# Performance work log

Hardware: AMD Instinct MI355X
Metric: run time of the kernel (lower is better)

The kernel has to match this reference:

```python
import jax, jax.numpy as jnp
import numpy as np
import math

B, C, N = 4, 128, 4096
GROUPS = 8
EPS = 1e-5


def setup_inputs() -> dict:
    key = jax.random.key(0)
    ks = jax.random.split(key, 7)
    x = jax.random.normal(ks[0], (B, C, N), dtype=jnp.float32)
    gn_w = jnp.ones((C,), dtype=jnp.float32)
    gn_b = jnp.zeros((C,), dtype=jnp.float32)
    # Conv1d with kernel_size=1 is a per-position linear map: weight [out, in]
    s_qkv = 1.0 / math.sqrt(C)
    w_qkv = jax.random.uniform(ks[1], (3 * C, C), jnp.float32, -s_qkv, s_qkv)
    b_qkv = jax.random.uniform(ks[2], (3 * C,), jnp.float32, -s_qkv, s_qkv)
    w_out = jax.random.uniform(ks[3], (C, C), jnp.float32, -s_qkv, s_qkv)
    b_out = jax.random.uniform(ks[4], (C,), jnp.float32, -s_qkv, s_qkv)
    return {"x": x, "gn_w": gn_w, "gn_b": gn_b, "w_qkv": w_qkv,
            "b_qkv": b_qkv, "w_out": w_out, "b_out": b_out}


def reference(x, gn_w, gn_b, w_qkv, b_qkv, w_out, b_out):
    b, c, n = x.shape
    # GroupNorm(8, c): normalize over (channels-in-group, n)
    xg = x.reshape(b, GROUPS, c // GROUPS, n)
    mean = jnp.mean(xg, axis=(2, 3), keepdims=True)
    var = jnp.var(xg, axis=(2, 3), keepdims=True)
    h = ((xg - mean) * jax.lax.rsqrt(var + EPS)).reshape(b, c, n)
    h = h * gn_w[None, :, None] + gn_b[None, :, None]
    # 1x1 conv QKV projection
    qkv = jnp.einsum('oc,bcn->bon', w_qkv, h) + b_qkv[None, :, None]
    q, k, v = jnp.split(qkv, 3, axis=1)  # each [b, c, n]
    scale = 1.0 / math.sqrt(c)
    attn = jax.nn.softmax(jnp.einsum('bci,bcj->bij', q, k) * scale, axis=-1)
    # h[b,c,i] = sum_j v[b,c,j] * attn[b,i,j]  (torch: bmm(v, attn^T))
    h2 = jnp.einsum('bcj,bij->bci', v, attn)
    out = jnp.einsum('oc,bcn->bon', w_out, h2) + b_out[None, :, None]
    return out + x
```

## Files before the change

kernel.cpp:

```cpp
#include <hip/hip_runtime.h>
#include <hip/hip_bf16.h>


#define CH 128
#define SEQ 4096
#define EPSV 1e-5f
#define QSCALE (0.08838834764831845f * 1.4426950408889634f)
#define SMAX 24.0f

typedef unsigned short u16;
typedef unsigned int u32;
typedef __attribute__((ext_vector_type(8))) short short8;
typedef __attribute__((ext_vector_type(4))) u32 u32x4;
typedef __attribute__((ext_vector_type(4))) float floatx4;
typedef __attribute__((ext_vector_type(16))) float floatx16;

__device__ __forceinline__ float bf2f(u16 h) {
    return __uint_as_float(((u32)h) << 16);
}
__device__ __forceinline__ float lo16(u32 wd) { return __uint_as_float(wd << 16); }
__device__ __forceinline__ float hi16(u32 wd) { return __uint_as_float(wd & 0xffff0000u); }
__device__ __forceinline__ u16 f2bf(float f) {
    u32 u = __float_as_uint(f);
    return (u16)((u + 0x7fffu + ((u >> 16) & 1u)) >> 16);
}
__device__ __forceinline__ u32 pkbf(float a, float b) {
    __hip_bfloat162 h = __float22bfloat162_rn(make_float2(a, b));
    u32 r;
    __builtin_memcpy(&r, &h, 4);
    return r;
}
__device__ __forceinline__ floatx4 mfma16(short8 a, short8 b, floatx4 c) {
    return __builtin_amdgcn_mfma_f32_16x16x32_bf16(a, b, c, 0, 0, 0);
}
__device__ __forceinline__ floatx16 mfma32(short8 a, short8 b, floatx16 c) {
    return __builtin_amdgcn_mfma_f32_32x32x16_bf16(a, b, c, 0, 0, 0);
}
__device__ __forceinline__ void pl32(u32& a, u32& b) {
    asm("v_permlane32_swap_b32 %0, %1" : "+v"(a), "+v"(b));
}
__device__ __forceinline__ short8 mk8(u32 a, u32 b, u32 c, u32 d) {
    u32x4 v = (u32x4){a, b, c, d};
    return __builtin_bit_cast(short8, v);
}

__global__ void gn_wconv(const float* __restrict__ x, float* __restrict__ part,
                         const float* __restrict__ w_qkv, const float* __restrict__ w_out,
                         u16* __restrict__ wq, u16* __restrict__ wo) {
    if (blockIdx.x >= 256) {
        int i = (blockIdx.x - 256) * 256 + threadIdx.x;
        if (i < 49152) wq[i] = f2bf(w_qkv[i]);
        else           wo[i - 49152] = f2bf(w_out[i - 49152]);
        return;
    }
    int bg = blockIdx.x >> 3, sub = blockIdx.x & 7;
    const float4* xp = (const float4*)(x + (size_t)bg * 65536 + sub * 8192);
    float s = 0.f, sq = 0.f;
    for (int r = 0; r < 8; ++r) {
        float4 v = xp[threadIdx.x + 256 * r];
        s  += v.x + v.y + v.z + v.w;
        sq += v.x*v.x + v.y*v.y + v.z*v.z + v.w*v.w;
    }
    for (int off = 32; off; off >>= 1) {
        s  += __shfl_down(s, off, 64);
        sq += __shfl_down(sq, off, 64);
    }
    __shared__ float ls[8];
    int wave = threadIdx.x >> 6, lane = threadIdx.x & 63;
    if (lane == 0) { ls[wave*2] = s; ls[wave*2+1] = sq; }
    __syncthreads();
    if (threadIdx.x == 0) {
        float ts = 0.f, tq = 0.f;
        for (int w = 0; w < 4; ++w) { ts += ls[w*2]; tq += ls[w*2+1]; }
        part[blockIdx.x * 2]     = ts;
        part[blockIdx.x * 2 + 1] = tq;
    }
}

__global__ __launch_bounds__(256, 2) void qkv_fused(
        const float* __restrict__ x, const float* __restrict__ gw,
        const float* __restrict__ gb, const float* __restrict__ part,
        const u16* __restrict__ wq, const float* __restrict__ b_qkv,
        u16* __restrict__ qT, u16* __restrict__ kT, u16* __restrict__ v) {
    __shared__ __align__(16) u16 hT[32 * 136];
    __shared__ __align__(16) u16 qbuf[32 * 132];
    __shared__ __align__(16) u16 kbuf[32 * 132];
    __shared__ __align__(16) u16 vbuf[128 * 36];
    __shared__ float cw[128], cb[128];
    int bx = blockIdx.x;
    int nc = bx & 127, b = bx >> 7;
    int n0 = nc * 32;
    int t = threadIdx.x, w = t >> 6, lane = t & 63;
    int quad = lane >> 4, l15 = lane & 15;

    if (t < 128) {
        int g = t >> 4;
        float s = 0.f, sq = 0.f;
        #pragma unroll
        for (int u = 0; u < 8; ++u) {
            s  += part[((b * 8 + g) * 8 + u) * 2];
            sq += part[((b * 8 + g) * 8 + u) * 2 + 1];
        }
        float mean = s / 65536.f;
        float rstd = rsqrtf(sq / 65536.f - mean * mean + EPSV);
        float wgt = gw[t] * rstd;
        cw[t] = wgt;
        cb[t] = gb[t] - mean * wgt;
    }

    short8 wf[6][4];
    float bqk[6];
    #pragma unroll
    for (int j = 0; j < 6; ++j) {
        int orow = (w * 6 + j) * 16 + l15;
        #pragma unroll
        for (int kt = 0; kt < 4; ++kt)
            wf[j][kt] = *(const short8*)(wq + orow * 128 + kt * 32 + quad * 8);
        bqk[j] = b_qkv[orow];
    }
    __syncthreads();

    #pragma unroll
    for (int r = 0; r < 4; ++r) {
        int u = r * 256 + t;
        int c = u >> 3, col = (u & 7) * 4;
        float wgt = cw[c], bs = cb[c];
        float4 xv = *(const float4*)(x + ((size_t)(b * 128 + c)) * SEQ + n0 + col);
        hT[(col + 0) * 136 + c] = f2bf(fmaf(xv.x, wgt, bs));
        hT[(col + 1) * 136 + c] = f2bf(fmaf(xv.y, wgt, bs));
        hT[(col + 2) * 136 + c] = f2bf(fmaf(xv.z, wgt, bs));
        hT[(col + 3) * 136 + c] = f2bf(fmaf(xv.w, wgt, bs));
    }
    __syncthreads();

    #pragma unroll
    for (int nt = 0; nt < 2; ++nt) {
        short8 hf[4];
        #pragma unroll
        for (int kt = 0; kt < 4; ++kt)
            hf[kt] = *(const short8*)(hT + (nt * 16 + l15) * 136 + kt * 32 + quad * 8);
        floatx4 acc[6];
        #pragma unroll
        for (int j = 0; j < 6; ++j) acc[j] = (floatx4)0.f;
        #pragma unroll
        for (int kt = 0; kt < 4; ++kt)
            #pragma unroll
            for (int j = 0; j < 6; ++j) {
                if (w * 6 + j < 16) acc[j] = mfma16(hf[kt], wf[j][kt], acc[j]);
                else                acc[j] = mfma16(wf[j][kt], hf[kt], acc[j]);
            }
        #pragma unroll
        for (int j = 0; j < 6; ++j) {
            int T = w * 6 + j;
            if (T < 8) {
                int o = T * 16 + l15;
                #pragma unroll
                for (int r = 0; r < 4; ++r)
                    qbuf[(nt * 16 + quad * 4 + r) * 132 + o] =
                        f2bf((acc[j][r] + bqk[j]) * QSCALE);
            } else if (T < 16) {
                int o = (T - 8) * 16 + l15;
                #pragma unroll
                for (int r = 0; r < 4; ++r)
                    kbuf[(nt * 16 + quad * 4 + r) * 132 + o] =
                        f2bf(acc[j][r] + bqk[j]);
            } else {
                #pragma unroll
                for (int r = 0; r < 4; ++r) {
                    int ov = (T - 16) * 16 + quad * 4 + r;
                    vbuf[ov * 36 + nt * 16 + l15] = f2bf(acc[j][r] + b_qkv[256 + ov]);
                }
            }
        }
    }
    __syncthreads();

    {
        u16* qg = qT + ((size_t)b * SEQ + n0) * CH;
        u16* kg = kT + ((size_t)b * SEQ + n0) * CH;
        #pragma unroll
        for (int rep = 0; rep < 2; ++rep) {
            int idx = rep * 256 + t;
            int n = idx >> 4, c8 = (idx & 15) * 8;
            *(uint4*)(qg + n * CH + c8) = *(const uint4*)(qbuf + n * 132 + c8);
            *(uint4*)(kg + n * CH + c8) = *(const uint4*)(kbuf + n * 132 + c8);
        }
        #pragma unroll
        for (int rep = 0; rep < 2; ++rep) {
            int idx = rep * 256 + t;
            int c = idx >> 2, n8 = (idx & 3) * 8;
            *(uint4*)(v + ((size_t)(b * CH + c)) * SEQ + n0 + n8) =
                *(const uint4*)(vbuf + c * 36 + n8);
        }
    }
}

__global__ __launch_bounds__(256, 2) void flash_attn(
        const u16* __restrict__ qT, const u16* __restrict__ kT,
        const u16* __restrict__ v, u16* __restrict__ partO,
        float* __restrict__ lbuf) {
    __shared__ __align__(16) char smem[71680];
    u16* qts = (u16*)(smem + 35840);
    u16* lds2 = (u16*)smem;

    int bx = blockIdx.x;
    int js = bx & 3, iblk = (bx >> 2) & 31, b = bx >> 7;
    int t = threadIdx.x, w = t >> 6, lane = t & 63;
    int il = lane & 31, h = lane >> 5;
    int i0 = iblk * 128, j0 = js * 1024;

    int tj = t >> 4, tc8 = (t & 15) * 8;
    int tv = t >> 3, vc8 = (t & 7) * 8;

    {
        const u16* qb = qT + ((size_t)b * SEQ + i0) * CH;
        for (int r = 0; r < 8; ++r) {
            int u = r * 256 + t;
            int i = u >> 4, c16 = u & 15;
            *(uint4*)(qts + i * 136 + c16 * 8) =
                *(const uint4*)(qb + (size_t)i * CH + c16 * 8);
        }
    }
    __syncthreads();
    short8 qf[8];
    #pragma unroll
    for (int kc = 0; kc < 8; ++kc)
        qf[kc] = *(const short8*)(qts + (w * 32 + il) * 136 + kc * 16 + h * 8);

    const u16* kTb = kT + ((size_t)b * SEQ + j0) * CH;
    const u16* vb  = v  + (size_t)b * CH * SEQ + j0;

    {
        u16* kts0 = (u16*)smem;
        u16* vts0 = kts0 + 8704;
        #pragma unroll
        for (int r = 0; r < 4; ++r)
            *(uint4*)(kts0 + (r * 16 + tj) * 136 + tc8) =
                *(const uint4*)(kTb + (size_t)(r * 16 + tj) * CH + tc8);
        #pragma unroll
        for (int r = 0; r < 4; ++r)
            *(uint4*)(vts0 + (r * 32 + tv) * 72 + vc8) =
                *(const uint4*)(vb + (size_t)(r * 32 + tv) * SEQ + vc8);
    }
    __syncthreads();

    float l_part = 0.f;
    floatx16 o[4];
    #pragma unroll
    for (int ct = 0; ct < 4; ++ct) o[ct] = (floatx16)0.f;

    for (int ch = 0; ch < 16; ++ch) {
        u16* kts = (u16*)(smem + (ch & 1) * 35840);
        u16* vts = kts + 8704;
        u16* ktsN = (u16*)(smem + ((ch + 1) & 1) * 35840);
        u16* vtsN = ktsN + 8704;
        int jb1 = (ch + 1) * 64;
        bool pf = (ch < 15);

        uint4 kreg[4];
        if (pf) {
            #pragma unroll
            for (int r = 0; r < 4; ++r)
                kreg[r] = *(const uint4*)(kTb + (size_t)(jb1 + r * 16 + tj) * CH + tc8);
        }

        short8 pfr[4];
        #pragma unroll
        for (int jt = 0; jt < 2; ++jt) {
            floatx16 s = (floatx16)(-SMAX);
            #pragma unroll
            for (int kc = 0; kc < 8; ++kc) {
                short8 kf = *(const short8*)(kts + (jt * 32 + il) * 136 + kc * 16 + h * 8);
                s = mfma32(kf, qf[kc], s);
            }
            float p[16];
            #pragma unroll
            for (int r = 0; r < 16; ++r) p[r] = __builtin_amdgcn_exp2f(s[r]);
            l_part += ((((p[0]+p[1])+(p[2]+p[3])) + ((p[4]+p[5])+(p[6]+p[7])))
                    +  (((p[8]+p[9])+(p[10]+p[11])) + ((p[12]+p[13])+(p[14]+p[15]))));
            u32 a0 = pkbf(p[0],  p[1]),  a1 = pkbf(p[2],  p[3]);
            u32 a2 = pkbf(p[4],  p[5]),  a3 = pkbf(p[6],  p[7]);
            u32 b0 = pkbf(p[8],  p[9]),  b1 = pkbf(p[10], p[11]);
            u32 b2 = pkbf(p[12], p[13]), b3 = pkbf(p[14], p[15]);
            pl32(a0, a2); pl32(a1, a3);
            pl32(b0, b2); pl32(b1, b3);
            pfr[2 * jt]     = mk8(a0, a1, a2, a3);
            pfr[2 * jt + 1] = mk8(b0, b1, b2, b3);
        }

        uint4 vreg[4];
        if (pf) {
            #pragma unroll
            for (int r = 0; r < 4; ++r)
                vreg[r] = *(const uint4*)(vb + (size_t)(r * 32 + tv) * SEQ + jb1 + vc8);
        }

        __builtin_amdgcn_s_setprio(1);
        #pragma unroll
        for (int ct = 0; ct < 4; ++ct) {
            const u16* vrow = vts + (ct * 32 + il) * 72;
            short8 vf0 = *(const short8*)(vrow + h * 8);
            short8 vf1 = *(const short8*)(vrow + 16 + h * 8);
            short8 vf2 = *(const short8*)(vrow + 32 + h * 8);
            short8 vf3 = *(const short8*)(vrow + 48 + h * 8);
            o[ct] = mfma32(vf0, pfr[0], o[ct]);
            o[ct] = mfma32(vf1, pfr[1], o[ct]);
            o[ct] = mfma32(vf2, pfr[2], o[ct]);
            o[ct] = mfma32(vf3, pfr[3], o[ct]);
        }
        __builtin_amdgcn_s_setprio(0);

        if (pf) {
            #pragma unroll
            for (int r = 0; r < 4; ++r)
                *(uint4*)(ktsN + (r * 16 + tj) * 136 + tc8) = kreg[r];
            #pragma unroll
            for (int r = 0; r < 4; ++r)
                *(uint4*)(vtsN + (r * 32 + tv) * 72 + vc8) = vreg[r];
        }
        __syncthreads();
    }

    #pragma unroll
    for (int ct = 0; ct < 4; ++ct)
        #pragma unroll
        for (int g = 0; g < 4; ++g) {
            uint2 pk2 = make_uint2(pkbf(o[ct][4*g+0], o[ct][4*g+1]),
                                   pkbf(o[ct][4*g+2], o[ct][4*g+3]));
            *(uint2*)(lds2 + (w * 32 + il) * 132 + ct * 32 + 8 * g + 4 * h) = pk2;
        }
    __syncthreads();
    int bi = b * 32 + iblk;
    u16* pb = partO + ((size_t)(js * 128 + bi)) * 16384;
    #pragma unroll
    for (int rep = 0; rep < 8; ++rep) {
        int idx = rep * 256 + t;
        int i = idx >> 4, c8 = (idx & 15) * 8;
        *(uint4*)(pb + i * 128 + c8) = *(const uint4*)(lds2 + i * 132 + c8);
    }
    l_part += __shfl_xor(l_part, 32, 64);
    if (lane < 32)
        lbuf[((size_t)(js * 128 + bi)) * 128 + w * 32 + il] = l_part;
}

__global__ __launch_bounds__(256, 2) void merge_out(
        const u16* __restrict__ partO, const float* __restrict__ lbuf,
        const u16* __restrict__ wo, const float* __restrict__ b_out,
        const float* __restrict__ x, float* __restrict__ out) {
    __shared__ __align__(16) u16 h2T[32 * 136];
    __shared__ float fac[32];
    int bx = blockIdx.x;
    int qtr = bx & 3, iblk = (bx >> 2) & 31, b = bx >> 7;
    int bi = b * 32 + iblk;
    int i_base = qtr * 32;
    int t = threadIdx.x, w = t >> 6, lane = t & 63;
    int quad = lane >> 4, l15 = lane & 15;

    short8 wf[2][4];
    #pragma unroll
    for (int j = 0; j < 2; ++j)
        #pragma unroll
        for (int kt = 0; kt < 4; ++kt)
            wf[j][kt] = *(const short8*)(wo + ((w * 2 + j) * 16 + l15) * 128 + kt * 32 + quad * 8);

    if (t < 32) {
        int i = i_base + t;
        float lv = 0.f;
        #pragma unroll
        for (int s = 0; s < 4; ++s)
            lv += lbuf[((size_t)(s * 128 + bi)) * 128 + i];
        fac[t] = 1.f / lv;
    }
    __syncthreads();

    {
        int il = t >> 3, oct = t & 7;
        int i = i_base + il;
        float accv[16];
        #pragma unroll
        for (int e = 0; e < 16; ++e) accv[e] = 0.f;
        for (int s = 0; s < 4; ++s) {
            const u16* pb = partO + ((size_t)(s * 128 + bi)) * 16384
                            + i * 128 + oct * 16;
            uint4 lo = *(const uint4*)(pb);
            uint4 hi = *(const uint4*)(pb + 8);
            accv[0]  += lo16(lo.x); accv[1]  += hi16(lo.x);
            accv[2]  += lo16(lo.y); accv[3]  += hi16(lo.y);
            accv[4]  += lo16(lo.z); accv[5]  += hi16(lo.z);
            accv[6]  += lo16(lo.w); accv[7]  += hi16(lo.w);
            accv[8]  += lo16(hi.x); accv[9]  += hi16(hi.x);
            accv[10] += lo16(hi.y); accv[11] += hi16(hi.y);
            accv[12] += lo16(hi.z); accv[13] += hi16(hi.z);
            accv[14] += lo16(hi.w); accv[15] += hi16(hi.w);
        }
        float fs = fac[il];
        #pragma unroll
        for (int e = 0; e < 16; ++e) accv[e] *= fs;
        uint4 lo = make_uint4(pkbf(accv[0],  accv[1]),  pkbf(accv[2],  accv[3]),
                              pkbf(accv[4],  accv[5]),  pkbf(accv[6],  accv[7]));
        uint4 hi = make_uint4(pkbf(accv[8],  accv[9]),  pkbf(accv[10], accv[11]),
                              pkbf(accv[12], accv[13]), pkbf(accv[14], accv[15]));
        *(uint4*)(h2T + il * 136 + oct * 16)     = lo;
        *(uint4*)(h2T + il * 136 + oct * 16 + 8) = hi;
    }
    __syncthreads();

    floatx4 acc[2][2];
    #pragma unroll
    for (int j = 0; j < 2; ++j) { acc[j][0] = (floatx4)0.f; acc[j][1] = (floatx4)0.f; }
    #pragma unroll
    for (int nt = 0; nt < 2; ++nt)
        #pragma unroll
        for (int kt = 0; kt < 4; ++kt) {
            short8 hf = *(const short8*)(h2T + (nt * 16 + l15) * 136 + kt * 32 + quad * 8);
            acc[0][nt] = mfma16(wf[0][kt], hf, acc[0][nt]);
            acc[1][nt] = mfma16(wf[1][kt], hf, acc[1][nt]);
        }

    int n_base = iblk * 128 + i_base;
    #pragma unroll
    for (int j = 0; j < 2; ++j)
        #pragma unroll
        for (int r = 0; r < 4; ++r) {
            int o = w * 32 + j * 16 + quad * 4 + r;
            float bo = b_out[o];
            #pragma unroll
            for (int nt = 0; nt < 2; ++nt) {
                int n = n_base + nt * 16 + l15;
                size_t idx = ((size_t)(b * 128 + o)) * SEQ + n;
                out[idx] = acc[j][nt][r] + bo + x[idx];
            }
        }
}

extern "C" void kernel_launch(void* const* d_in, const int* in_sizes, int n_in,
                              void* d_out, int out_size, void* d_ws, size_t ws_size,
                              hipStream_t stream) {
    const float* x     = (const float*)d_in[0];
    const float* gn_w  = (const float*)d_in[1];
    const float* gn_b  = (const float*)d_in[2];
    const float* w_qkv = (const float*)d_in[3];
    const float* b_qkv = (const float*)d_in[4];
    const float* w_out = (const float*)d_in[5];
    const float* b_out = (const float*)d_in[6];
    float* out = (float*)d_out;

    char* ws = (char*)d_ws;
    float* part = (float*)ws;
    u16*  wq  = (u16*)(ws + 4096);
    u16*  wo  = (u16*)(ws + 102400);
    u16*  qT  = (u16*)(ws + 135168);
    u16*  kT  = (u16*)(ws + 4329472);
    u16*  v   = (u16*)(ws + 8523776);
    u16*  pO  = (u16*)(ws + 12718080);
    float* lb = (float*)(ws + 29495296);

    gn_wconv<<<512, 256, 0, stream>>>(x, part, w_qkv, w_out, wq, wo);
    qkv_fused<<<512, 256, 0, stream>>>(x, gn_w, gn_b, part, wq, b_qkv, qT, kT, v);
    flash_attn<<<512, 256, 0, stream>>>(qT, kT, v, pO, lb);
    merge_out<<<512, 256, 0, stream>>>(pO, lb, wo, b_out, x, out);
}
```

Measured before the change: 69.20 us.

## Load V fragments directly from global memory instead of staging in LDS

The flash-attention kernel no longer stages V tiles through shared memory. Each wave now loads its MFMA V operands straight from global memory into registers, issuing them interleaved with the QK and PV MFMAs, and the LDS footprint drops to just the double-buffered K tiles (Q staging reuses the same region, with an extra barrier added). The aim is to remove the LDS round trip and its bank traffic for V and to allow more resident blocks. The cost is redundant, less coalesced global reads of V across the four waves, with load latency exposed directly to the MFMA chain.

```diff
diff --git a/kernel.cpp b/kernel.cpp
--- a/kernel.cpp
+++ b/kernel.cpp
@@ -199,8 +199,8 @@
         const u16* __restrict__ qT, const u16* __restrict__ kT,
         const u16* __restrict__ v, u16* __restrict__ partO,
         float* __restrict__ lbuf) {
-    __shared__ __align__(16) char smem[71680];
-    u16* qts = (u16*)(smem + 35840);
+    __shared__ __align__(16) char smem[34816];
+    u16* qts = (u16*)smem;
     u16* lds2 = (u16*)smem;
 
     int bx = blockIdx.x;
@@ -210,7 +210,6 @@
     int i0 = iblk * 128, j0 = js * 1024;
 
     int tj = t >> 4, tc8 = (t & 15) * 8;
-    int tv = t >> 3, vc8 = (t & 7) * 8;
 
     {
         const u16* qb = qT + ((size_t)b * SEQ + i0) * CH;
@@ -226,21 +225,17 @@
     #pragma unroll
     for (int kc = 0; kc < 8; ++kc)
         qf[kc] = *(const short8*)(qts + (w * 32 + il) * 136 + kc * 16 + h * 8);
+    __syncthreads();
 
     const u16* kTb = kT + ((size_t)b * SEQ + j0) * CH;
     const u16* vb  = v  + (size_t)b * CH * SEQ + j0;
 
     {
         u16* kts0 = (u16*)smem;
-        u16* vts0 = kts0 + 8704;
         #pragma unroll
         for (int r = 0; r < 4; ++r)
             *(uint4*)(kts0 + (r * 16 + tj) * 136 + tc8) =
                 *(const uint4*)(kTb + (size_t)(r * 16 + tj) * CH + tc8);
-        #pragma unroll
-        for (int r = 0; r < 4; ++r)
-            *(uint4*)(vts0 + (r * 32 + tv) * 72 + vc8) =
-                *(const uint4*)(vb + (size_t)(r * 32 + tv) * SEQ + vc8);
     }
     __syncthreads();
 
@@ -249,13 +244,20 @@
     #pragma unroll
     for (int ct = 0; ct < 4; ++ct) o[ct] = (floatx16)0.f;
 
+#define LDV(dst, vbc, ct) do {                                           \
+        const u16* _vr = (vbc) + (size_t)((ct) * 32 + il) * SEQ;         \
+        dst[0] = *(const short8*)(_vr + h * 8);                          \
+        dst[1] = *(const short8*)(_vr + 16 + h * 8);                     \
+        dst[2] = *(const short8*)(_vr + 32 + h * 8);                     \
+        dst[3] = *(const short8*)(_vr + 48 + h * 8);                     \
+    } while (0)
+
     for (int ch = 0; ch < 16; ++ch) {
-        u16* kts = (u16*)(smem + (ch & 1) * 35840);
-        u16* vts = kts + 8704;
-        u16* ktsN = (u16*)(smem + ((ch + 1) & 1) * 35840);
-        u16* vtsN = ktsN + 8704;
+        u16* kts = (u16*)(smem + (ch & 1) * 17408);
+        u16* ktsN = (u16*)(smem + ((ch + 1) & 1) * 17408);
         int jb1 = (ch + 1) * 64;
         bool pf = (ch < 15);
+        const u16* vbc = vb + ch * 64;
 
         uint4 kreg[4];
         if (pf) {
@@ -265,12 +267,13 @@
         }
 
         short8 pfr[4];
-        #pragma unroll
-        for (int jt = 0; jt < 2; ++jt) {
+        short8 va[4], vy[4];
+
+        {
             floatx16 s = (floatx16)(-SMAX);
             #pragma unroll
             for (int kc = 0; kc < 8; ++kc) {
-                short8 kf = *(const short8*)(kts + (jt * 32 + il) * 136 + kc * 16 + h * 8);
+                short8 kf = *(const short8*)(kts + il * 136 + kc * 16 + h * 8);
                 s = mfma32(kf, qf[kc], s);
             }
             float p[16];
@@ -284,42 +287,62 @@
             u32 b2 = pkbf(p[12], p[13]), b3 = pkbf(p[14], p[15]);
             pl32(a0, a2); pl32(a1, a3);
             pl32(b0, b2); pl32(b1, b3);
-            pfr[2 * jt]     = mk8(a0, a1, a2, a3);
-            pfr[2 * jt + 1] = mk8(b0, b1, b2, b3);
-        }
-
-        uint4 vreg[4];
-        if (pf) {
-            #pragma unroll
-            for (int r = 0; r < 4; ++r)
-                vreg[r] = *(const uint4*)(vb + (size_t)(r * 32 + tv) * SEQ + jb1 + vc8);
+            pfr[0] = mk8(a0, a1, a2, a3);
+            pfr[1] = mk8(b0, b1, b2, b3);
+        }
+        {
+            floatx16 s = (floatx16)(-SMAX);
+            #pragma unroll
+            for (int kc = 0; kc < 8; ++kc) {
+                short8 kf = *(const short8*)(kts + (32 + il) * 136 + kc * 16 + h * 8);
+                s = mfma32(kf, qf[kc], s);
+            }
+            LDV(va, vbc, 0);
+            LDV(vy, vbc, 1);
+            float p[16];
+            #pragma unroll
+            for (int r = 0; r < 16; ++r) p[r] = __builtin_amdgcn_exp2f(s[r]);
+            l_part += ((((p[0]+p[1])+(p[2]+p[3])) + ((p[4]+p[5])+(p[6]+p[7])))
+                    +  (((p[8]+p[9])+(p[10]+p[11])) + ((p[12]+p[13])+(p[14]+p[15]))));
+            u32 a0 = pkbf(p[0],  p[1]),  a1 = pkbf(p[2],  p[3]);
+            u32 a2 = pkbf(p[4],  p[5]),  a3 = pkbf(p[6],  p[7]);
+            u32 b0 = pkbf(p[8],  p[9]),  b1 = pkbf(p[10], p[11]);
+            u32 b2 = pkbf(p[12], p[13]), b3 = pkbf(p[14], p[15]);
+            pl32(a0, a2); pl32(a1, a3);
+            pl32(b0, b2); pl32(b1, b3);
+            pfr[2] = mk8(a0, a1, a2, a3);
+            pfr[3] = mk8(b0, b1, b2, b3);
         }
 
         __builtin_amdgcn_s_setprio(1);
-        #pragma unroll
-        for (int ct = 0; ct < 4; ++ct) {
-            const u16* vrow = vts + (ct * 32 + il) * 72;
-            short8 vf0 = *(const short8*)(vrow + h * 8);
-            short8 vf1 = *(const short8*)(vrow + 16 + h * 8);
-            short8 vf2 = *(const short8*)(vrow + 32 + h * 8);
-            short8 vf3 = *(const short8*)(vrow + 48 + h * 8);
-            o[ct] = mfma32(vf0, pfr[0], o[ct]);
-            o[ct] = mfma32(vf1, pfr[1], o[ct]);
-            o[ct] = mfma32(vf2, pfr[2], o[ct]);
-            o[ct] = mfma32(vf3, pfr[3], o[ct]);
-        }
+        o[0] = mfma32(va[0], pfr[0], o[0]);
+        o[0] = mfma32(va[1], pfr[1], o[0]);
+        o[0] = mfma32(va[2], pfr[2], o[0]);
+        o[0] = mfma32(va[3], pfr[3], o[0]);
+        LDV(va, vbc, 2);
+        o[1] = mfma32(vy[0], pfr[0], o[1]);
+        o[1] = mfma32(vy[1], pfr[1], o[1]);
+        o[1] = mfma32(vy[2], pfr[2], o[1]);
+        o[1] = mfma32(vy[3], pfr[3], o[1]);
+        LDV(vy, vbc, 3);
+        o[2] = mfma32(va[0], pfr[0], o[2]);
+        o[2] = mfma32(va[1], pfr[1], o[2]);
+        o[2] = mfma32(va[2], pfr[2], o[2]);
+        o[2] = mfma32(va[3], pfr[3], o[2]);
+        o[3] = mfma32(vy[0], pfr[0], o[3]);
+        o[3] = mfma32(vy[1], pfr[1], o[3]);
+        o[3] = mfma32(vy[2], pfr[2], o[3]);
+        o[3] = mfma32(vy[3], pfr[3], o[3]);
         __builtin_amdgcn_s_setprio(0);
 
         if (pf) {
             #pragma unroll
             for (int r = 0; r < 4; ++r)
                 *(uint4*)(ktsN + (r * 16 + tj) * 136 + tc8) = kreg[r];
-            #pragma unroll
-            for (int r = 0; r < 4; ++r)
-                *(uint4*)(vtsN + (r * 32 + tv) * 72 + vc8) = vreg[r];
         }
         __syncthreads();
     }
+#undef LDV
 
     #pragma unroll
     for (int ct = 0; ct < 4; ++ct)
```

New measurement: 108.4 us. 1.57x slower.
